# Kernel tuning notes

Measured on AMD Instinct MI355X. Metric: run time of the kernel, lower is better.

## Reference

```python
import jax, jax.numpy as jnp
import numpy as np


def _next_fast_len(n):
    # smallest 5-smooth integer >= n (matches scipy.fftpack.next_fast_len)
    while True:
        m = n
        for p in (2, 3, 5):
            while m % p == 0:
                m //= p
        if m == 1:
            return n
        n += 1


def _conv1d_fft(values, weights):
    # values: [b, h, n, d], weights: [h, m]; FFT cross-correlation implementing
    # causal exponentially-decaying weighted sum (per-head EMA of values).
    N = values.shape[-2]
    M = weights.shape[-1]
    L = _next_fast_len(N + M - 1)
    f_v = jnp.fft.rfft(values, n=L, axis=-2)          # [b,h,F,d] complex
    f_w = jnp.fft.rfft(weights, n=L, axis=-1)         # [h,F]   complex
    out = jnp.fft.irfft(f_v * jnp.conj(f_w)[..., None], n=L, axis=-2)
    out = jnp.roll(out, -1, axis=-2)
    return out[..., L - N:, :]                         # [b,h,N,d]


def setup_inputs() -> dict:
    key = jax.random.key(0)
    ks = jax.random.split(key, 7)
    B, N, D, H = 4, 8192, 512, 8
    s = 1.0 / np.sqrt(D)
    return {
        "x": jax.random.normal(ks[0], (B, N, D), dtype=jnp.float32),
        "W_in": jax.random.normal(ks[1], (D, D), dtype=jnp.float32) * s,
        "b_in": jax.random.normal(ks[2], (D,), dtype=jnp.float32) * 0.01,
        "W_out": jax.random.normal(ks[3], (D, D), dtype=jnp.float32) * s,
        "b_out": jax.random.normal(ks[4], (D,), dtype=jnp.float32) * 0.01,
        "init_state": jax.random.normal(ks[5], (H, D // H), dtype=jnp.float32),
        "alpha_param": jax.random.normal(ks[6], (H,), dtype=jnp.float32),
    }


def reference(x, W_in, b_in, W_out, b_out, init_state, alpha_param):
    B, N, D = x.shape
    H, Dh = init_state.shape
    # input projection
    xp = x @ W_in.T + b_in                             # [B,N,D]
    xh = xp.reshape(B, N, H, Dh).transpose(0, 2, 1, 3)  # [B,H,N,Dh]
    # prepend learned init state, take first differences along time
    x0 = jnp.broadcast_to(init_state[None, :, None, :], (B, H, 1, Dh))
    xc = jnp.concatenate([x0, xh], axis=2)             # [B,H,N+1,Dh]
    xd = xc[:, :, 1:] - xc[:, :, :-1]                  # [B,H,N,Dh]
    # per-head smoothing coefficients
    alpha = jax.nn.sigmoid(alpha_param)[:, None]       # [H,1]
    ar = jnp.arange(N, dtype=x.dtype)
    weights = alpha * (1.0 - alpha) ** ar[::-1]        # [H,N]
    out = _conv1d_fft(xd, weights)                     # [B,H,N,Dh]
    # contribution of the initial state
    init_w = (1.0 - alpha) ** (ar + 1.0)               # [H,N]
    out = out + init_w[:, :, None] * init_state[:, None, :]
    out = out.transpose(0, 2, 1, 3).reshape(B, N, D)
    return out @ W_out.T + b_out
```

## Files before the change

### kernel.cpp

```cpp
#include <hip/hip_runtime.h>
#include <stdint.h>

#define SEQ      8192
#define BATCH    4
#define DIM      512
#define MROWS    32768
#define CHUNK    64
#define NCHUNK   128
#define NCHAN    2048
#define NHEAD    8
#define NGCHUNK  512
#define XLD      264
#define NITER    16

typedef unsigned short ushort;
typedef unsigned int   uint;
typedef __bf16 bf16x8 __attribute__((ext_vector_type(8)));
typedef float  f32x4  __attribute__((ext_vector_type(4)));
typedef ushort usx8   __attribute__((ext_vector_type(8)));

__device__ __forceinline__ ushort f2bf(float f) {
    union { __bf16 h; ushort u; } cv;
    cv.h = (__bf16)f;
    return cv.u;
}
__device__ __forceinline__ float bf2f(ushort v) {
    return __uint_as_float(((unsigned)v) << 16);
}

__global__ void weights_to_bf16_kernel(const float* __restrict__ w_in,
                                       const float* __restrict__ w_out,
                                       ushort* __restrict__ dst, int n4each) {
    int i = blockIdx.x * blockDim.x + threadIdx.x;
    if (i >= 2 * n4each) return;
    const float4* src = (i < n4each) ? (const float4*)w_in
                                     : (const float4*)w_out - n4each;
    float4 v = src[i];
    ushort4 r;
    r.x = f2bf(v.x); r.y = f2bf(v.y); r.z = f2bf(v.z); r.w = f2bf(v.w);
    ((ushort4*)dst)[i] = r;
}

#define GLDS(g, l) __builtin_amdgcn_global_load_lds(                        \
        (const __attribute__((address_space(1))) void*)(g),                 \
        (__attribute__((address_space(3))) void*)(l), 16, 0, 0)

#define WAITV(n)  asm volatile("s_waitcnt vmcnt(" #n ")" ::: "memory")
#define WAITL0()  asm volatile("s_waitcnt lgkmcnt(0)" ::: "memory")
#define BAR()     do { __builtin_amdgcn_s_barrier();                        \
                       __builtin_amdgcn_sched_barrier(0); } while (0)
#define SBAR()    __builtin_amdgcn_sched_barrier(0)


__global__ __launch_bounds__(512, 4) void gemm1_scan_kernel(
        const float* __restrict__ x,    const ushort* __restrict__ Bw,
        const float* __restrict__ b_in, const float* __restrict__ alpha_param,
        ushort* __restrict__ zout,
        float* __restrict__ Lfin,       float* __restrict__ XpT)
{
    __shared__ __align__(16) char smem[73728];
    ushort* As0 = (ushort*)smem;
    ushort* Bs0 = (ushort*)(smem + 24576);
    ushort* X   = (ushort*)smem;

    const int tid = threadIdx.x;
    const int bn  = blockIdx.x;
    const int bm  = blockIdx.y;

    const int lane = tid & 63;
    const int wave = tid >> 6;
    const int wr = wave >> 2, wc = wave & 3;
    const int quad = lane >> 4, r16 = lane & 15;

    const int srow  = tid >> 2;
    const int ks    = tid & 3;
    const int rx    = (srow >> 1) & 3;
    const int skoff = ks * 8;
    const float*  Ag  = x  + (size_t)(bm * 128 + srow) * DIM + skoff;
    const ushort* Bg0 = Bw + (size_t)(bn * 256 + srow) * DIM + ((ks ^ rx) << 3);
    const ushort* Bg1 = Bg0 + (size_t)128 * DIM;
    const int aWrOff = srow * 32 + ((ks ^ rx) << 3);

    f32x4 acc[4][4];
    #pragma unroll
    for (int i = 0; i < 4; i++)
        #pragma unroll
        for (int j = 0; j < 4; j++)
            acc[i][j] = f32x4{0.f, 0.f, 0.f, 0.f};

    auto stageB = [&](int k0, int b) {
        GLDS(Bg0 + k0, &Bs0[b * 8192 + tid * 8]);
        GLDS(Bg1 + k0, &Bs0[b * 8192 + 4096 + tid * 8]);
    };
    auto packA = [&](float4 lo, float4 hi) {
        usx8 w;
        w[0] = f2bf(lo.x); w[1] = f2bf(lo.y); w[2] = f2bf(lo.z); w[3] = f2bf(lo.w);
        w[4] = f2bf(hi.x); w[5] = f2bf(hi.y); w[6] = f2bf(hi.z); w[7] = f2bf(hi.w);
        return w;
    };

    float4 aLo0, aHi0, aLo1, aHi1;

    aLo0 = *(const float4*)(Ag);      aHi0 = *(const float4*)(Ag + 4);
    stageB(0, 0);
    aLo1 = *(const float4*)(Ag + 32); aHi1 = *(const float4*)(Ag + 36);
    stageB(32, 1);
    *(usx8*)&As0[aWrOff] = packA(aLo0, aHi0);

    const int rxr = (r16 >> 1) & 3;

    #pragma unroll
    for (int k = 0; k < NITER; ++k) {
        const int cur = k % 3;
        const int stg = (k + 2) % 3;
        const int wnx = (k + 1) % 3;

        if (k + 1 < NITER) {
            usx8 w = ((k & 1) == 0) ? packA(aLo1, aHi1) : packA(aLo0, aHi0);
            *(usx8*)&As0[wnx * 4096 + aWrOff] = w;
        }
        if (k < NITER - 1) WAITV(4); else WAITV(0);
        WAITL0();
        BAR();

        if (k + 2 < NITER) {
            const int ko = (k + 2) * 32;
            if ((k & 1) == 0) {
                aLo0 = *(const float4*)(Ag + ko); aHi0 = *(const float4*)(Ag + ko + 4);
            } else {
                aLo1 = *(const float4*)(Ag + ko); aHi1 = *(const float4*)(Ag + ko + 4);
            }
            SBAR();
            stageB(ko, stg);
        }

        bf16x8 af[4], bfr[4];
        #pragma unroll
        for (int i = 0; i < 4; i++)
            af[i] = *(const bf16x8*)&As0[cur * 4096 + (wr * 64 + i * 16 + r16) * 32
                                         + ((quad ^ rxr) << 3)];
        #pragma unroll
        for (int j = 0; j < 4; j++)
            bfr[j] = *(const bf16x8*)&Bs0[cur * 8192 + (wc * 64 + j * 16 + r16) * 32
                                          + ((quad ^ rxr) << 3)];

        #pragma unroll
        for (int i = 0; i < 4; i++)
            #pragma unroll
            for (int j = 0; j < 4; j++)
                acc[i][j] = __builtin_amdgcn_mfma_f32_16x16x32_bf16(
                                bfr[j], af[i], acc[i][j], 0, 0, 0);
    }

    __syncthreads();
    #pragma unroll
    for (int i = 0; i < 4; i++) {
        const int ml = wr * 64 + i * 16 + r16;
        #pragma unroll
        for (int j = 0; j < 4; j++) {
            const int nl = wc * 64 + j * 16 + quad * 4;
            const float4 bv = *(const float4*)&b_in[bn * 256 + nl];
            ushort4 r4;
            r4.x = f2bf(acc[i][j][0] + bv.x);
            r4.y = f2bf(acc[i][j][1] + bv.y);
            r4.z = f2bf(acc[i][j][2] + bv.z);
            r4.w = f2bf(acc[i][j][3] + bv.w);
            *(ushort4*)&X[ml * XLD + nl] = r4;
        }
    }
    __syncthreads();

    const int chalf = tid >> 8;
    const int cidx  = tid & 255;
    const int g     = 2 * bm + chalf;
    const int d     = bn * 256 + cidx;
    const int h     = d >> 6;
    const float alpha = 1.0f / (1.0f + expf(-alpha_param[h]));
    const float c     = 1.0f - alpha;

    const ushort* Xr  = X + chalf * 64 * XLD + cidx;
    ushort* zrow = zout + ((size_t)(bm * 128 + chalf * 64)) * DIM + d;

    float z = 0.f, prev = 0.f;
    #pragma unroll 8
    for (int r = 0; r < CHUNK; ++r) {
        float xv = bf2f(Xr[r * XLD]);
        z = c * z + alpha * (xv - prev);
        prev = xv;
        zrow[(size_t)r * DIM] = f2bf(z);
    }
    Lfin[(size_t)g * 512 + d]       = z;
    XpT[(size_t)(g + 1) * 512 + d]  = prev;
}

__global__ void scan_fixg_kernel(const float* __restrict__ Lfin,
                                 const float* __restrict__ XpT,
                                 const float* __restrict__ alpha_param,
                                 const float* __restrict__ init_state,
                                 float* __restrict__ G)
{
    int ch = blockIdx.x * blockDim.x + threadIdx.x;
    if (ch >= NCHAN) return;
    const int b = ch >> 9;
    const int d = ch & (DIM - 1);
    const int h = d >> 6;
    const float alpha = 1.0f / (1.0f + expf(-alpha_param[h]));
    const float c = 1.0f - alpha;
    const float c2 = c * c, c4 = c2 * c2, c8 = c4 * c4,
                c16 = c8 * c8, c32 = c16 * c16;
    const float c63 = c32 * c16 * c8 * c4 * c2 * c;
    const float sinit = init_state[d];

    float Z = sinit;
    const float* Lp = Lfin + (size_t)(b * NCHUNK) * 512 + d;
    const float* Xp = XpT  + (size_t)(b * NCHUNK) * 512 + d;
    float*       Gp = G    + (size_t)(b * NCHUNK) * 512 + d;

    constexpr int PF = 16;
    float Lr[PF], Xr[PF];
    #pragma unroll
    for (int j = 0; j < PF; ++j) {
        Lr[j] = Lp[(size_t)j * 512];
        Xr[j] = Xp[(size_t)j * 512];
    }
    for (int gr = 0; gr < NCHUNK / PF; ++gr) {
        #pragma unroll
        for (int j = 0; j < PF; ++j) {
            const int kl = gr * PF + j;
            const float xpt = (kl == 0) ? sinit : Xr[j];
            const float Lc  = Lr[j];
            if (gr + 1 < NCHUNK / PF) {
                Lr[j] = Lp[(size_t)((gr + 1) * PF + j) * 512];
                Xr[j] = Xp[(size_t)((gr + 1) * PF + j) * 512];
            }
            const float Gv = c * Z - alpha * xpt;
            Gp[(size_t)kl * 512] = Gv;
            Z = Lc + c63 * Gv;
        }
    }
}

__global__ __launch_bounds__(512, 4) void gemm2_kernel(
        const ushort* __restrict__ Az, const ushort* __restrict__ Bw,
        const float* __restrict__ bias, float* __restrict__ Cout,
        const float* __restrict__ G, const float* __restrict__ alpha_param)
{
    __shared__ __align__(16) char smem[73728];
    ushort* As0 = (ushort*)smem;
    ushort* Bs0 = (ushort*)(smem + 24576);

    const int tid  = threadIdx.x;
    const int lane = tid & 63;
    const int wave = tid >> 6;
    const int wr = wave >> 2, wc = wave & 3;
    const int bm = blockIdx.y, bn = blockIdx.x;
    const int quad = lane >> 4, r16 = lane & 15;

    const int srow  = tid >> 2;
    const int ks    = tid & 3;
    const int rx    = (srow >> 1) & 3;
    const int skoff = ks * 8;
    const ushort* Ag16 = Az + (size_t)(bm * 128 + srow) * DIM + skoff;
    const ushort* Bg0  = Bw + (size_t)(bn * 256 + srow) * DIM + ((ks ^ rx) << 3);
    const ushort* Bg1  = Bg0 + (size_t)128 * DIM;
    const int aWrOff = srow * 32 + ((ks ^ rx) << 3);

    const int m   = bm * 128 + srow;
    const int tau = m & (CHUNK - 1);
    const float* Gc = G + (size_t)(m >> 6) * 512;
    const float t1 = (float)tau;
    float fc0,fc1,fc2,fc3,fc4,fc5,fc6,fc7;
    {
        float a, c;
        a = 1.f/(1.f+expf(-alpha_param[0])); c = 1.f - a; fc0 = exp2f(t1 * log2f(c));
        a = 1.f/(1.f+expf(-alpha_param[1])); c = 1.f - a; fc1 = exp2f(t1 * log2f(c));
        a = 1.f/(1.f+expf(-alpha_param[2])); c = 1.f - a; fc2 = exp2f(t1 * log2f(c));
        a = 1.f/(1.f+expf(-alpha_param[3])); c = 1.f - a; fc3 = exp2f(t1 * log2f(c));
        a = 1.f/(1.f+expf(-alpha_param[4])); c = 1.f - a; fc4 = exp2f(t1 * log2f(c));
        a = 1.f/(1.f+expf(-alpha_param[5])); c = 1.f - a; fc5 = exp2f(t1 * log2f(c));
        a = 1.f/(1.f+expf(-alpha_param[6])); c = 1.f - a; fc6 = exp2f(t1 * log2f(c));
        a = 1.f/(1.f+expf(-alpha_param[7])); c = 1.f - a; fc7 = exp2f(t1 * log2f(c));
    }
    auto selfac = [&](int hh) -> float {
        float f = fc0;
        f = (hh == 1) ? fc1 : f;
        f = (hh == 2) ? fc2 : f;
        f = (hh == 3) ? fc3 : f;
        f = (hh == 4) ? fc4 : f;
        f = (hh == 5) ? fc5 : f;
        f = (hh == 6) ? fc6 : f;
        f = (hh == 7) ? fc7 : f;
        return f;
    };
    auto fixpack = [&](usx8 av, float4 z0, float4 z1, float fac) {
        usx8 w;
        w[0] = f2bf(bf2f(av[0]) + fac * z0.x);
        w[1] = f2bf(bf2f(av[1]) + fac * z0.y);
        w[2] = f2bf(bf2f(av[2]) + fac * z0.z);
        w[3] = f2bf(bf2f(av[3]) + fac * z0.w);
        w[4] = f2bf(bf2f(av[4]) + fac * z1.x);
        w[5] = f2bf(bf2f(av[5]) + fac * z1.y);
        w[6] = f2bf(bf2f(av[6]) + fac * z1.z);
        w[7] = f2bf(bf2f(av[7]) + fac * z1.w);
        return w;
    };

    f32x4 acc[4][4];
    #pragma unroll
    for (int i = 0; i < 4; i++)
        #pragma unroll
        for (int j = 0; j < 4; j++)
            acc[i][j] = f32x4{0.f, 0.f, 0.f, 0.f};

    auto stageB = [&](int k0, int b) {
        GLDS(Bg0 + k0, &Bs0[b * 8192 + tid * 8]);
        GLDS(Bg1 + k0, &Bs0[b * 8192 + 4096 + tid * 8]);
    };

    usx8 av0, av1; float4 g0lo, g0hi, g1lo, g1hi;

    av0 = *(const usx8*)(Ag16);
    g0lo = *(const float4*)&Gc[skoff]; g0hi = *(const float4*)&Gc[skoff + 4];
    stageB(0, 0);
    av1 = *(const usx8*)(Ag16 + 32);
    g1lo = *(const float4*)&Gc[32 + skoff]; g1hi = *(const float4*)&Gc[32 + skoff + 4];
    stageB(32, 1);
    *(usx8*)&As0[aWrOff] = fixpack(av0, g0lo, g0hi, selfac(skoff >> 6));

    const int rxr = (r16 >> 1) & 3;

    #pragma unroll
    for (int k = 0; k < NITER; ++k) {
        const int cur = k % 3;
        const int stg = (k + 2) % 3;
        const int wnx = (k + 1) % 3;

        if (k + 1 < NITER) {
            const float fac = selfac((((k + 1) * 32) + skoff) >> 6);
            usx8 w = ((k & 1) == 0) ? fixpack(av1, g1lo, g1hi, fac)
                                    : fixpack(av0, g0lo, g0hi, fac);
            *(usx8*)&As0[wnx * 4096 + aWrOff] = w;
        }
        if (k < NITER - 1) WAITV(5); else WAITV(0);
        WAITL0();
        BAR();

        if (k + 2 < NITER) {
            const int ko = (k + 2) * 32;
            if ((k & 1) == 0) {
                av0 = *(const usx8*)(Ag16 + ko);
                g0lo = *(const float4*)&Gc[ko + skoff];
                g0hi = *(const float4*)&Gc[ko + skoff + 4];
            } else {
                av1 = *(const usx8*)(Ag16 + ko);
                g1lo = *(const float4*)&Gc[ko + skoff];
                g1hi = *(const float4*)&Gc[ko + skoff + 4];
            }
            SBAR();
            stageB(ko, stg);
        }

        bf16x8 af[4], bfr[4];
        #pragma unroll
        for (int i = 0; i < 4; i++)
            af[i] = *(const bf16x8*)&As0[cur * 4096 + (wr * 64 + i * 16 + r16) * 32
                                         + ((quad ^ rxr) << 3)];
        #pragma unroll
        for (int j = 0; j < 4; j++)
            bfr[j] = *(const bf16x8*)&Bs0[cur * 8192 + (wc * 64 + j * 16 + r16) * 32
                                          + ((quad ^ rxr) << 3)];

        #pragma unroll
        for (int i = 0; i < 4; i++)
            #pragma unroll
            for (int j = 0; j < 4; j++)
                acc[i][j] = __builtin_amdgcn_mfma_f32_16x16x32_bf16(
                                bfr[j], af[i], acc[i][j], 0, 0, 0);
    }

    #pragma unroll
    for (int i = 0; i < 4; i++) {
        const int mr = bm * 128 + wr * 64 + i * 16 + r16;
        #pragma unroll
        for (int j = 0; j < 4; j++) {
            const int n0 = bn * 256 + wc * 64 + j * 16 + quad * 4;
            const float4 bv = *(const float4*)&bias[n0];
            float4 v = make_float4(acc[i][j][0] + bv.x, acc[i][j][1] + bv.y,
                                   acc[i][j][2] + bv.z, acc[i][j][3] + bv.w);
            *(float4*)&Cout[(size_t)mr * DIM + n0] = v;
        }
    }
}

extern "C" void kernel_launch(void* const* d_in, const int* in_sizes, int n_in,
                              void* d_out, int out_size, void* d_ws, size_t ws_size,
                              hipStream_t stream) {
    const float* x           = (const float*)d_in[0];
    const float* W_in        = (const float*)d_in[1];
    const float* b_in        = (const float*)d_in[2];
    const float* W_out       = (const float*)d_in[3];
    const float* b_out       = (const float*)d_in[4];
    const float* init_state  = (const float*)d_in[5];
    const float* alpha_param = (const float*)d_in[6];
    float* out = (float*)d_out;

    ushort* z_bf    = (ushort*)d_ws;
    ushort* win_bf  = z_bf   + (size_t)MROWS * DIM;
    ushort* wout_bf = win_bf + (size_t)DIM * DIM;
    float*  Lfin    = (float*)(wout_bf + (size_t)DIM * DIM);
    float*  XpT     = Lfin + (size_t)NGCHUNK * 512;
    float*  G       = XpT  + (size_t)(NGCHUNK + 1) * 512;

    const int nw4 = (DIM * DIM) / 4;
    weights_to_bf16_kernel<<<(2 * nw4 + 255) / 256, 256, 0, stream>>>(
        W_in, W_out, win_bf, nw4);

    dim3 g1(2, MROWS / 128);
    gemm1_scan_kernel<<<g1, 512, 0, stream>>>(
        x, win_bf, b_in, alpha_param, z_bf, Lfin, XpT);

    scan_fixg_kernel<<<NCHAN / 256, 256, 0, stream>>>(
        Lfin, XpT, alpha_param, init_state, G);

    dim3 g2(2, MROWS / 128);
    gemm2_kernel<<<g2, 512, 0, stream>>>(
        z_bf, wout_bf, b_out, out, G, alpha_param);
}
```

Before: 175.3 us.

## Shrink GEMM tiles to 128x128 with 256 threads, double-buffer, and swizzle tile order

Both GEMM kernels move from 128x256 tiles with 512 threads and triple buffering to 128x128 tiles with 256 threads and double buffering. Tile order is remapped for better L2 locality, the G correction rows are staged into LDS once per block, and the MFMA section gets raised wave priority. The aim is more blocks in flight and less LDS per block, at the cost of more total A reloads and a changed sync pattern.

```diff
diff --git a/kernel.cpp b/kernel.cpp
--- a/kernel.cpp
+++ b/kernel.cpp
@@ -8,9 +8,8 @@
 #define CHUNK    64
 #define NCHUNK   128
 #define NCHAN    2048
-#define NHEAD    8
 #define NGCHUNK  512
-#define XLD      264
+#define XLD      136
 #define NITER    16
 
 typedef unsigned short ushort;
@@ -51,35 +50,44 @@
                        __builtin_amdgcn_sched_barrier(0); } while (0)
 #define SBAR()    __builtin_amdgcn_sched_barrier(0)
 
-
-__global__ __launch_bounds__(512, 4) void gemm1_scan_kernel(
+__device__ __forceinline__ void tile_decode(int& bm, int& bn) {
+    const int orig = blockIdx.y * gridDim.x + blockIdx.x;
+    const int tl   = (orig & 7) * 128 + (orig >> 3);
+    bm = tl >> 2; bn = tl & 3;
+}
+
+
+__global__ __launch_bounds__(256, 4) void gemm1_scan_kernel(
         const float* __restrict__ x,    const ushort* __restrict__ Bw,
         const float* __restrict__ b_in, const float* __restrict__ alpha_param,
         ushort* __restrict__ zout,
         float* __restrict__ Lfin,       float* __restrict__ XpT)
 {
-    __shared__ __align__(16) char smem[73728];
+    __shared__ __align__(16) char smem[34816];
     ushort* As0 = (ushort*)smem;
-    ushort* Bs0 = (ushort*)(smem + 24576);
+    ushort* Bs0 = (ushort*)(smem + 16384);
     ushort* X   = (ushort*)smem;
 
     const int tid = threadIdx.x;
-    const int bn  = blockIdx.x;
-    const int bm  = blockIdx.y;
+    int bm, bn; tile_decode(bm, bn);
 
     const int lane = tid & 63;
     const int wave = tid >> 6;
-    const int wr = wave >> 2, wc = wave & 3;
+    const int wr = wave >> 1, wc = wave & 1;
     const int quad = lane >> 4, r16 = lane & 15;
 
-    const int srow  = tid >> 2;
-    const int ks    = tid & 3;
-    const int rx    = (srow >> 1) & 3;
-    const int skoff = ks * 8;
-    const float*  Ag  = x  + (size_t)(bm * 128 + srow) * DIM + skoff;
-    const ushort* Bg0 = Bw + (size_t)(bn * 256 + srow) * DIM + ((ks ^ rx) << 3);
-    const ushort* Bg1 = Bg0 + (size_t)128 * DIM;
-    const int aWrOff = srow * 32 + ((ks ^ rx) << 3);
+    const int brow = tid >> 2;
+    const int bslot = tid & 3;
+    const int brx = (brow >> 1) & 3;
+    const ushort* Bg0 = Bw + (size_t)(bn * 128 + brow) * DIM + ((bslot ^ brx) << 3);
+    const ushort* Bg1 = Bg0 + (size_t)64 * DIM;
+
+    const int srow  = tid >> 1;
+    const int skoff = (tid & 1) * 16;
+    const int arx   = (srow >> 1) & 3;
+    const float* Ag = x + (size_t)(bm * 128 + srow) * DIM + skoff;
+    const int aw0 = srow * 32 + (((2 * (tid & 1) + 0) ^ arx) << 3);
+    const int aw1 = srow * 32 + (((2 * (tid & 1) + 1) ^ arx) << 3);
 
     f32x4 acc[4][4];
     #pragma unroll
@@ -89,67 +97,76 @@
             acc[i][j] = f32x4{0.f, 0.f, 0.f, 0.f};
 
     auto stageB = [&](int k0, int b) {
-        GLDS(Bg0 + k0, &Bs0[b * 8192 + tid * 8]);
-        GLDS(Bg1 + k0, &Bs0[b * 8192 + 4096 + tid * 8]);
+        GLDS(Bg0 + k0, &Bs0[b * 4096 + tid * 8]);
+        GLDS(Bg1 + k0, &Bs0[b * 4096 + 2048 + tid * 8]);
     };
-    auto packA = [&](float4 lo, float4 hi) {
+    auto cvt8 = [&](float4 lo, float4 hi) {
         usx8 w;
         w[0] = f2bf(lo.x); w[1] = f2bf(lo.y); w[2] = f2bf(lo.z); w[3] = f2bf(lo.w);
         w[4] = f2bf(hi.x); w[5] = f2bf(hi.y); w[6] = f2bf(hi.z); w[7] = f2bf(hi.w);
         return w;
     };
 
-    float4 aLo0, aHi0, aLo1, aHi1;
-
-    aLo0 = *(const float4*)(Ag);      aHi0 = *(const float4*)(Ag + 4);
+    float4 a00, a01, a02, a03, a10, a11, a12, a13;
+
     stageB(0, 0);
-    aLo1 = *(const float4*)(Ag + 32); aHi1 = *(const float4*)(Ag + 36);
-    stageB(32, 1);
-    *(usx8*)&As0[aWrOff] = packA(aLo0, aHi0);
+    a00 = *(const float4*)(Ag);      a01 = *(const float4*)(Ag + 4);
+    a02 = *(const float4*)(Ag + 8);  a03 = *(const float4*)(Ag + 12);
+    a10 = *(const float4*)(Ag + 32); a11 = *(const float4*)(Ag + 36);
+    a12 = *(const float4*)(Ag + 40); a13 = *(const float4*)(Ag + 44);
+    *(usx8*)&As0[aw0] = cvt8(a00, a01);
+    *(usx8*)&As0[aw1] = cvt8(a02, a03);
+    WAITV(4); WAITL0(); BAR();
 
     const int rxr = (r16 >> 1) & 3;
 
     #pragma unroll
     for (int k = 0; k < NITER; ++k) {
-        const int cur = k % 3;
-        const int stg = (k + 2) % 3;
-        const int wnx = (k + 1) % 3;
-
-        if (k + 1 < NITER) {
-            usx8 w = ((k & 1) == 0) ? packA(aLo1, aHi1) : packA(aLo0, aHi0);
-            *(usx8*)&As0[wnx * 4096 + aWrOff] = w;
-        }
-        if (k < NITER - 1) WAITV(4); else WAITV(0);
-        WAITL0();
-        BAR();
-
+        const int cb = k & 1, nb = cb ^ 1;
+
+        if (k + 1 < NITER) stageB((k + 1) * 32, nb);
         if (k + 2 < NITER) {
             const int ko = (k + 2) * 32;
             if ((k & 1) == 0) {
-                aLo0 = *(const float4*)(Ag + ko); aHi0 = *(const float4*)(Ag + ko + 4);
+                a00 = *(const float4*)(Ag + ko);      a01 = *(const float4*)(Ag + ko + 4);
+                a02 = *(const float4*)(Ag + ko + 8);  a03 = *(const float4*)(Ag + ko + 12);
             } else {
-                aLo1 = *(const float4*)(Ag + ko); aHi1 = *(const float4*)(Ag + ko + 4);
+                a10 = *(const float4*)(Ag + ko);      a11 = *(const float4*)(Ag + ko + 4);
+                a12 = *(const float4*)(Ag + ko + 8);  a13 = *(const float4*)(Ag + ko + 12);
             }
-            SBAR();
-            stageB(ko, stg);
+        }
+        if (k + 1 < NITER) {
+            if ((k & 1) == 0) {
+                *(usx8*)&As0[nb * 4096 + aw0] = cvt8(a10, a11);
+                *(usx8*)&As0[nb * 4096 + aw1] = cvt8(a12, a13);
+            } else {
+                *(usx8*)&As0[nb * 4096 + aw0] = cvt8(a00, a01);
+                *(usx8*)&As0[nb * 4096 + aw1] = cvt8(a02, a03);
+            }
         }
 
         bf16x8 af[4], bfr[4];
         #pragma unroll
         for (int i = 0; i < 4; i++)
-            af[i] = *(const bf16x8*)&As0[cur * 4096 + (wr * 64 + i * 16 + r16) * 32
+            af[i] = *(const bf16x8*)&As0[cb * 4096 + (wr * 64 + i * 16 + r16) * 32
                                          + ((quad ^ rxr) << 3)];
         #pragma unroll
         for (int j = 0; j < 4; j++)
-            bfr[j] = *(const bf16x8*)&Bs0[cur * 8192 + (wc * 64 + j * 16 + r16) * 32
+            bfr[j] = *(const bf16x8*)&Bs0[cb * 4096 + (wc * 64 + j * 16 + r16) * 32
                                           + ((quad ^ rxr) << 3)];
-
+        WAITL0();
+        SBAR();
+        __builtin_amdgcn_s_setprio(1);
         #pragma unroll
         for (int i = 0; i < 4; i++)
             #pragma unroll
             for (int j = 0; j < 4; j++)
                 acc[i][j] = __builtin_amdgcn_mfma_f32_16x16x32_bf16(
                                 bfr[j], af[i], acc[i][j], 0, 0, 0);
+        __builtin_amdgcn_s_setprio(0);
+
+        if (k < NITER - 2) WAITV(4); else WAITV(0);
+        BAR();
     }
 
     __syncthreads();
@@ -159,7 +176,7 @@
         #pragma unroll
         for (int j = 0; j < 4; j++) {
             const int nl = wc * 64 + j * 16 + quad * 4;
-            const float4 bv = *(const float4*)&b_in[bn * 256 + nl];
+            const float4 bv = *(const float4*)&b_in[bn * 128 + nl];
             ushort4 r4;
             r4.x = f2bf(acc[i][j][0] + bv.x);
             r4.y = f2bf(acc[i][j][1] + bv.y);
@@ -170,10 +187,10 @@
     }
     __syncthreads();
 
-    const int chalf = tid >> 8;
-    const int cidx  = tid & 255;
+    const int chalf = tid >> 7;
+    const int cidx  = tid & 127;
     const int g     = 2 * bm + chalf;
-    const int d     = bn * 256 + cidx;
+    const int d     = bn * 128 + cidx;
     const int h     = d >> 6;
     const float alpha = 1.0f / (1.0f + expf(-alpha_param[h]));
     const float c     = 1.0f - alpha;
@@ -240,35 +257,39 @@
     }
 }
 
-__global__ __launch_bounds__(512, 4) void gemm2_kernel(
+__global__ __launch_bounds__(256, 4) void gemm2_kernel(
         const ushort* __restrict__ Az, const ushort* __restrict__ Bw,
         const float* __restrict__ bias, float* __restrict__ Cout,
         const float* __restrict__ G, const float* __restrict__ alpha_param)
 {
-    __shared__ __align__(16) char smem[73728];
+    __shared__ __align__(16) char smem[36864];
     ushort* As0 = (ushort*)smem;
-    ushort* Bs0 = (ushort*)(smem + 24576);
-
-    const int tid  = threadIdx.x;
+    ushort* Bs0 = (ushort*)(smem + 16384);
+    float*  Gl  = (float*)(smem + 32768);
+
+    const int tid = threadIdx.x;
+    int bm, bn; tile_decode(bm, bn);
+
     const int lane = tid & 63;
     const int wave = tid >> 6;
-    const int wr = wave >> 2, wc = wave & 3;
-    const int bm = blockIdx.y, bn = blockIdx.x;
+    const int wr = wave >> 1, wc = wave & 1;
     const int quad = lane >> 4, r16 = lane & 15;
 
-    const int srow  = tid >> 2;
-    const int ks    = tid & 3;
-    const int rx    = (srow >> 1) & 3;
-    const int skoff = ks * 8;
+    const int brow = tid >> 2;
+    const int bslot = tid & 3;
+    const int brx = (brow >> 1) & 3;
+    const ushort* Bg0 = Bw + (size_t)(bn * 128 + brow) * DIM + ((bslot ^ brx) << 3);
+    const ushort* Bg1 = Bg0 + (size_t)64 * DIM;
+
+    const int srow  = tid >> 1;
+    const int skoff = (tid & 1) * 16;
+    const int arx   = (srow >> 1) & 3;
     const ushort* Ag16 = Az + (size_t)(bm * 128 + srow) * DIM + skoff;
-    const ushort* Bg0  = Bw + (size_t)(bn * 256 + srow) * DIM + ((ks ^ rx) << 3);
-    const ushort* Bg1  = Bg0 + (size_t)128 * DIM;
-    const int aWrOff = srow * 32 + ((ks ^ rx) << 3);
-
-    const int m   = bm * 128 + srow;
-    const int tau = m & (CHUNK - 1);
-    const float* Gc = G + (size_t)(m >> 6) * 512;
-    const float t1 = (float)tau;
+    const int aw0 = srow * 32 + (((2 * (tid & 1) + 0) ^ arx) << 3);
+    const int aw1 = srow * 32 + (((2 * (tid & 1) + 1) ^ arx) << 3);
+    const int grow = srow >> 6;
+
+    const float t1 = (float)(srow & 63);
     float fc0,fc1,fc2,fc3,fc4,fc5,fc6,fc7;
     {
         float a, c;
@@ -292,18 +313,6 @@
         f = (hh == 7) ? fc7 : f;
         return f;
     };
-    auto fixpack = [&](usx8 av, float4 z0, float4 z1, float fac) {
-        usx8 w;
-        w[0] = f2bf(bf2f(av[0]) + fac * z0.x);
-        w[1] = f2bf(bf2f(av[1]) + fac * z0.y);
-        w[2] = f2bf(bf2f(av[2]) + fac * z0.z);
-        w[3] = f2bf(bf2f(av[3]) + fac * z0.w);
-        w[4] = f2bf(bf2f(av[4]) + fac * z1.x);
-        w[5] = f2bf(bf2f(av[5]) + fac * z1.y);
-        w[6] = f2bf(bf2f(av[6]) + fac * z1.z);
-        w[7] = f2bf(bf2f(av[7]) + fac * z1.w);
-        return w;
-    };
 
     f32x4 acc[4][4];
     #pragma unroll
@@ -313,69 +322,89 @@
             acc[i][j] = f32x4{0.f, 0.f, 0.f, 0.f};
 
     auto stageB = [&](int k0, int b) {
-        GLDS(Bg0 + k0, &Bs0[b * 8192 + tid * 8]);
-        GLDS(Bg1 + k0, &Bs0[b * 8192 + 4096 + tid * 8]);
+        GLDS(Bg0 + k0, &Bs0[b * 4096 + tid * 8]);
+        GLDS(Bg1 + k0, &Bs0[b * 4096 + 2048 + tid * 8]);
     };
-
-    usx8 av0, av1; float4 g0lo, g0hi, g1lo, g1hi;
-
-    av0 = *(const usx8*)(Ag16);
-    g0lo = *(const float4*)&Gc[skoff]; g0hi = *(const float4*)&Gc[skoff + 4];
+    auto writeFixed = [&](int nb, usx8 z0, usx8 z1, int dbase) {
+        const float fac = selfac(dbase >> 6);
+        float4 gA = *(const float4*)&Gl[grow * 512 + dbase];
+        float4 gB = *(const float4*)&Gl[grow * 512 + dbase + 4];
+        float4 gC = *(const float4*)&Gl[grow * 512 + dbase + 8];
+        float4 gD = *(const float4*)&Gl[grow * 512 + dbase + 12];
+        usx8 w0, w1;
+        w0[0] = f2bf(bf2f(z0[0]) + fac * gA.x);
+        w0[1] = f2bf(bf2f(z0[1]) + fac * gA.y);
+        w0[2] = f2bf(bf2f(z0[2]) + fac * gA.z);
+        w0[3] = f2bf(bf2f(z0[3]) + fac * gA.w);
+        w0[4] = f2bf(bf2f(z0[4]) + fac * gB.x);
+        w0[5] = f2bf(bf2f(z0[5]) + fac * gB.y);
+        w0[6] = f2bf(bf2f(z0[6]) + fac * gB.z);
+        w0[7] = f2bf(bf2f(z0[7]) + fac * gB.w);
+        w1[0] = f2bf(bf2f(z1[0]) + fac * gC.x);
+        w1[1] = f2bf(bf2f(z1[1]) + fac * gC.y);
+        w1[2] = f2bf(bf2f(z1[2]) + fac * gC.z);
+        w1[3] = f2bf(bf2f(z1[3]) + fac * gC.w);
+        w1[4] = f2bf(bf2f(z1[4]) + fac * gD.x);
+        w1[5] = f2bf(bf2f(z1[5]) + fac * gD.y);
+        w1[6] = f2bf(bf2f(z1[6]) + fac * gD.z);
+        w1[7] = f2bf(bf2f(z1[7]) + fac * gD.w);
+        *(usx8*)&As0[nb * 4096 + aw0] = w0;
+        *(usx8*)&As0[nb * 4096 + aw1] = w1;
+    };
+
+    usx8 z00, z01, z10, z11;
+
+    GLDS((const float*)G + (size_t)bm * 1024 + tid * 4, (char*)Gl + tid * 16);
     stageB(0, 0);
-    av1 = *(const usx8*)(Ag16 + 32);
-    g1lo = *(const float4*)&Gc[32 + skoff]; g1hi = *(const float4*)&Gc[32 + skoff + 4];
-    stageB(32, 1);
-    *(usx8*)&As0[aWrOff] = fixpack(av0, g0lo, g0hi, selfac(skoff >> 6));
+    z00 = *(const usx8*)(Ag16);      z01 = *(const usx8*)(Ag16 + 8);
+    z10 = *(const usx8*)(Ag16 + 32); z11 = *(const usx8*)(Ag16 + 40);
+    WAITV(6);
+    writeFixed(0, z00, z01, skoff);
+    WAITV(2); WAITL0(); BAR();
 
     const int rxr = (r16 >> 1) & 3;
 
     #pragma unroll
     for (int k = 0; k < NITER; ++k) {
-        const int cur = k % 3;
-        const int stg = (k + 2) % 3;
-        const int wnx = (k + 1) % 3;
-
-        if (k + 1 < NITER) {
-            const float fac = selfac((((k + 1) * 32) + skoff) >> 6);
-            usx8 w = ((k & 1) == 0) ? fixpack(av1, g1lo, g1hi, fac)
-                                    : fixpack(av0, g0lo, g0hi, fac);
-            *(usx8*)&As0[wnx * 4096 + aWrOff] = w;
-        }
-        if (k < NITER - 1) WAITV(5); else WAITV(0);
-        WAITL0();
-        BAR();
-
+        const int cb = k & 1, nb = cb ^ 1;
+
+        if (k + 1 < NITER) stageB((k + 1) * 32, nb);
         if (k + 2 < NITER) {
             const int ko = (k + 2) * 32;
             if ((k & 1) == 0) {
-                av0 = *(const usx8*)(Ag16 + ko);
-                g0lo = *(const float4*)&Gc[ko + skoff];
-                g0hi = *(const float4*)&Gc[ko + skoff + 4];
+                z00 = *(const usx8*)(Ag16 + ko); z01 = *(const usx8*)(Ag16 + ko + 8);
             } else {
-                av1 = *(const usx8*)(Ag16 + ko);
-                g1lo = *(const float4*)&Gc[ko + skoff];
-                g1hi = *(const float4*)&Gc[ko + skoff + 4];
+                z10 = *(const usx8*)(Ag16 + ko); z11 = *(const usx8*)(Ag16 + ko + 8);
             }
-            SBAR();
-            stageB(ko, stg);
+        }
+        if (k + 1 < NITER) {
+            const int dbase = (k + 1) * 32 + skoff;
+            if ((k & 1) == 0) writeFixed(nb, z10, z11, dbase);
+            else              writeFixed(nb, z00, z01, dbase);
         }
 
         bf16x8 af[4], bfr[4];
         #pragma unroll
         for (int i = 0; i < 4; i++)
-            af[i] = *(const bf16x8*)&As0[cur * 4096 + (wr * 64 + i * 16 + r16) * 32
+            af[i] = *(const bf16x8*)&As0[cb * 4096 + (wr * 64 + i * 16 + r16) * 32
                                          + ((quad ^ rxr) << 3)];
         #pragma unroll
         for (int j = 0; j < 4; j++)
-            bfr[j] = *(const bf16x8*)&Bs0[cur * 8192 + (wc * 64 + j * 16 + r16) * 32
+            bfr[j] = *(const bf16x8*)&Bs0[cb * 4096 + (wc * 64 + j * 16 + r16) * 32
                                           + ((quad ^ rxr) << 3)];
-
+        WAITL0();
+        SBAR();
+        __builtin_amdgcn_s_setprio(1);
         #pragma unroll
         for (int i = 0; i < 4; i++)
             #pragma unroll
             for (int j = 0; j < 4; j++)
                 acc[i][j] = __builtin_amdgcn_mfma_f32_16x16x32_bf16(
                                 bfr[j], af[i], acc[i][j], 0, 0, 0);
+        __builtin_amdgcn_s_setprio(0);
+
+        if (k < NITER - 2) WAITV(2); else WAITV(0);
+        BAR();
     }
 
     #pragma unroll
@@ -383,7 +412,7 @@
         const int mr = bm * 128 + wr * 64 + i * 16 + r16;
         #pragma unroll
         for (int j = 0; j < 4; j++) {
-            const int n0 = bn * 256 + wc * 64 + j * 16 + quad * 4;
+            const int n0 = bn * 128 + wc * 64 + j * 16 + quad * 4;
             const float4 bv = *(const float4*)&bias[n0];
             float4 v = make_float4(acc[i][j][0] + bv.x, acc[i][j][1] + bv.y,
                                    acc[i][j][2] + bv.z, acc[i][j][3] + bv.w);
@@ -415,14 +444,14 @@
     weights_to_bf16_kernel<<<(2 * nw4 + 255) / 256, 256, 0, stream>>>(
         W_in, W_out, win_bf, nw4);
 
-    dim3 g1(2, MROWS / 128);
-    gemm1_scan_kernel<<<g1, 512, 0, stream>>>(
+    dim3 g1(DIM / 128, MROWS / 128);
+    gemm1_scan_kernel<<<g1, 256, 0, stream>>>(
         x, win_bf, b_in, alpha_param, z_bf, Lfin, XpT);
 
     scan_fixg_kernel<<<NCHAN / 256, 256, 0, stream>>>(
         Lfin, XpT, alpha_param, init_state, G);
 
-    dim3 g2(2, MROWS / 128);
-    gemm2_kernel<<<g2, 512, 0, stream>>>(
+    dim3 g2(DIM / 128, MROWS / 128);
+    gemm2_kernel<<<g2, 256, 0, stream>>>(
         z_bf, wout_bf, b_out, out, G, alpha_param);
 }
```

New measurement: 187.9 us. 7.2% more time.

## Deepen A-operand register prefetch to three stages and remap tile order

Applied to the files above, without the earlier changes.

Both GEMM kernels now prefetch the A operand (fp32 x, or bf16 z plus G corrections) three k-steps ahead into a triple set of registers instead of two, with vmcnt waits recomputed per iteration. Block indices are also remapped through a decode that interleaves the linear block ID across eight groups, changing which M/N tiles run concurrently for L2/locality. The deeper prefetch is meant to hide global-load latency better, at the cost of more VGPRs, which may pressure occupancy at 4 waves/SIMD.

```diff
diff --git a/kernel.cpp b/kernel.cpp
--- a/kernel.cpp
+++ b/kernel.cpp
@@ -8,7 +8,6 @@
 #define CHUNK    64
 #define NCHUNK   128
 #define NCHAN    2048
-#define NHEAD    8
 #define NGCHUNK  512
 #define XLD      264
 #define NITER    16
@@ -51,6 +50,12 @@
                        __builtin_amdgcn_sched_barrier(0); } while (0)
 #define SBAR()    __builtin_amdgcn_sched_barrier(0)
 
+__device__ __forceinline__ void tile_decode(int& bm, int& bn) {
+    const int orig = blockIdx.y * gridDim.x + blockIdx.x;
+    const int tl   = (orig & 7) * 64 + (orig >> 3);
+    bm = tl >> 1; bn = tl & 1;
+}
+
 
 __global__ __launch_bounds__(512, 4) void gemm1_scan_kernel(
         const float* __restrict__ x,    const ushort* __restrict__ Bw,
@@ -64,8 +69,7 @@
     ushort* X   = (ushort*)smem;
 
     const int tid = threadIdx.x;
-    const int bn  = blockIdx.x;
-    const int bm  = blockIdx.y;
+    int bm, bn; tile_decode(bm, bn);
 
     const int lane = tid & 63;
     const int wave = tid >> 6;
@@ -99,13 +103,14 @@
         return w;
     };
 
-    float4 aLo0, aHi0, aLo1, aHi1;
-
-    aLo0 = *(const float4*)(Ag);      aHi0 = *(const float4*)(Ag + 4);
+    float4 aL0, aH0, aL1, aH1, aL2, aH2;
+
+    aL0 = *(const float4*)(Ag);      aH0 = *(const float4*)(Ag + 4);
+    aL1 = *(const float4*)(Ag + 32); aH1 = *(const float4*)(Ag + 36);
+    aL2 = *(const float4*)(Ag + 64); aH2 = *(const float4*)(Ag + 68);
     stageB(0, 0);
-    aLo1 = *(const float4*)(Ag + 32); aHi1 = *(const float4*)(Ag + 36);
     stageB(32, 1);
-    *(usx8*)&As0[aWrOff] = packA(aLo0, aHi0);
+    *(usx8*)&As0[aWrOff] = packA(aL0, aH0);
 
     const int rxr = (r16 >> 1) & 3;
 
@@ -116,23 +121,27 @@
         const int wnx = (k + 1) % 3;
 
         if (k + 1 < NITER) {
-            usx8 w = ((k & 1) == 0) ? packA(aLo1, aHi1) : packA(aLo0, aHi0);
+            usx8 w;
+            if (wnx == 0)      w = packA(aL0, aH0);
+            else if (wnx == 1) w = packA(aL1, aH1);
+            else               w = packA(aL2, aH2);
             *(usx8*)&As0[wnx * 4096 + aWrOff] = w;
         }
-        if (k < NITER - 1) WAITV(4); else WAITV(0);
+        if (k == 0)       WAITV(2);
+        else if (k <= 13) WAITV(4);
+        else if (k == 14) WAITV(2);
+        else              WAITV(0);
         WAITL0();
         BAR();
 
-        if (k + 2 < NITER) {
-            const int ko = (k + 2) * 32;
-            if ((k & 1) == 0) {
-                aLo0 = *(const float4*)(Ag + ko); aHi0 = *(const float4*)(Ag + ko + 4);
-            } else {
-                aLo1 = *(const float4*)(Ag + ko); aHi1 = *(const float4*)(Ag + ko + 4);
-            }
-            SBAR();
-            stageB(ko, stg);
-        }
+        if (k + 3 < NITER) {
+            const int ko = (k + 3) * 32;
+            if (cur == 0)      { aL0 = *(const float4*)(Ag + ko); aH0 = *(const float4*)(Ag + ko + 4); }
+            else if (cur == 1) { aL1 = *(const float4*)(Ag + ko); aH1 = *(const float4*)(Ag + ko + 4); }
+            else               { aL2 = *(const float4*)(Ag + ko); aH2 = *(const float4*)(Ag + ko + 4); }
+        }
+        SBAR();
+        if (k + 2 < NITER) stageB((k + 2) * 32, stg);
 
         bf16x8 af[4], bfr[4];
         #pragma unroll
@@ -249,11 +258,12 @@
     ushort* As0 = (ushort*)smem;
     ushort* Bs0 = (ushort*)(smem + 24576);
 
-    const int tid  = threadIdx.x;
+    const int tid = threadIdx.x;
+    int bm, bn; tile_decode(bm, bn);
+
     const int lane = tid & 63;
     const int wave = tid >> 6;
     const int wr = wave >> 2, wc = wave & 3;
-    const int bm = blockIdx.y, bn = blockIdx.x;
     const int quad = lane >> 4, r16 = lane & 15;
 
     const int srow  = tid >> 2;
@@ -266,9 +276,8 @@
     const int aWrOff = srow * 32 + ((ks ^ rx) << 3);
 
     const int m   = bm * 128 + srow;
-    const int tau = m & (CHUNK - 1);
     const float* Gc = G + (size_t)(m >> 6) * 512;
-    const float t1 = (float)tau;
+    const float t1 = (float)(m & (CHUNK - 1));
     float fc0,fc1,fc2,fc3,fc4,fc5,fc6,fc7;
     {
         float a, c;
@@ -317,15 +326,17 @@
         GLDS(Bg1 + k0, &Bs0[b * 8192 + 4096 + tid * 8]);
     };
 
-    usx8 av0, av1; float4 g0lo, g0hi, g1lo, g1hi;
+    usx8 av0, av1, av2; float4 g0l, g0h, g1l, g1h, g2l, g2h;
 
     av0 = *(const usx8*)(Ag16);
-    g0lo = *(const float4*)&Gc[skoff]; g0hi = *(const float4*)&Gc[skoff + 4];
+    g0l = *(const float4*)&Gc[skoff];      g0h = *(const float4*)&Gc[skoff + 4];
+    av1 = *(const usx8*)(Ag16 + 32);
+    g1l = *(const float4*)&Gc[32 + skoff]; g1h = *(const float4*)&Gc[32 + skoff + 4];
+    av2 = *(const usx8*)(Ag16 + 64);
+    g2l = *(const float4*)&Gc[64 + skoff]; g2h = *(const float4*)&Gc[64 + skoff + 4];
     stageB(0, 0);
-    av1 = *(const usx8*)(Ag16 + 32);
-    g1lo = *(const float4*)&Gc[32 + skoff]; g1hi = *(const float4*)&Gc[32 + skoff + 4];
     stageB(32, 1);
-    *(usx8*)&As0[aWrOff] = fixpack(av0, g0lo, g0hi, selfac(skoff >> 6));
+    *(usx8*)&As0[aWrOff] = fixpack(av0, g0l, g0h, selfac(skoff >> 6));
 
     const int rxr = (r16 >> 1) & 3;
 
@@ -337,28 +348,34 @@
 
         if (k + 1 < NITER) {
             const float fac = selfac((((k + 1) * 32) + skoff) >> 6);
-            usx8 w = ((k & 1) == 0) ? fixpack(av1, g1lo, g1hi, fac)
-                                    : fixpack(av0, g0lo, g0hi, fac);
+            usx8 w;
+            if (wnx == 0)      w = fixpack(av0, g0l, g0h, fac);
+            else if (wnx == 1) w = fixpack(av1, g1l, g1h, fac);
+            else               w = fixpack(av2, g2l, g2h, fac);
             *(usx8*)&As0[wnx * 4096 + aWrOff] = w;
         }
-        if (k < NITER - 1) WAITV(5); else WAITV(0);
+        if (k == 0)       WAITV(2);
+        else if (k <= 13) WAITV(5);
+        else if (k == 14) WAITV(2);
+        else              WAITV(0);
         WAITL0();
         BAR();
 
-        if (k + 2 < NITER) {
-            const int ko = (k + 2) * 32;
-            if ((k & 1) == 0) {
+        if (k + 3 < NITER) {
+            const int ko = (k + 3) * 32;
+            if (cur == 0) {
                 av0 = *(const usx8*)(Ag16 + ko);
-                g0lo = *(const float4*)&Gc[ko + skoff];
-                g0hi = *(const float4*)&Gc[ko + skoff + 4];
+                g0l = *(const float4*)&Gc[ko + skoff]; g0h = *(const float4*)&Gc[ko + skoff + 4];
+            } else if (cur == 1) {
+                av1 = *(const usx8*)(Ag16 + ko);
+                g1l = *(const float4*)&Gc[ko + skoff]; g1h = *(const float4*)&Gc[ko + skoff + 4];
             } else {
-                av1 = *(const usx8*)(Ag16 + ko);
-                g1lo = *(const float4*)&Gc[ko + skoff];
-                g1hi = *(const float4*)&Gc[ko + skoff + 4];
+                av2 = *(const usx8*)(Ag16 + ko);
+                g2l = *(const float4*)&Gc[ko + skoff]; g2h = *(const float4*)&Gc[ko + skoff + 4];
             }
-            SBAR();
-            stageB(ko, stg);
-        }
+        }
+        SBAR();
+        if (k + 2 < NITER) stageB((k + 2) * 32, stg);
 
         bf16x8 af[4], bfr[4];
         #pragma unroll
```

Result: slower. 180.7 us (+3.1%).
